# Kernel tuning notes

Measured on AMD Instinct MI355X. Metric: run time of the kernel, lower is better.

## Reference

```python
import jax, jax.numpy as jnp
import numpy as np

R, A, E, K, NREL = 2048, 16384, 131072, 48, 7
RADIUS = 10.0


def setup_inputs():
    key = jax.random.key(0)
    ks = jax.random.split(key, 20)
    f = jax.random.normal
    return {
        "node_feature": f(ks[0], (R, 21), jnp.float32),
        "all_atom_pos": f(ks[1], (A, 3), jnp.float32) * 8.0,
        "atom_name": jax.random.randint(ks[2], (A,), 0, 38),
        "ca_idx": jax.random.randint(ks[3], (R,), 0, A),
        "edge_src": jax.random.randint(ks[4], (E,), 0, R),
        "edge_dst": jax.random.randint(ks[5], (E,), 0, R),
        "edge_rel": jax.random.randint(ks[6], (E,), 0, NREL),
        # parameters (atom-type embedding table, residue-type linear, AEP point MLP,
        # relational graph conv, env2structures MLP with BN)
        "emb_atom": f(ks[7], (39, 64), jnp.float32) * 0.02,
        "Wres": f(ks[8], (21, 64), jnp.float32) * 0.1,
        "bres": jnp.zeros((64,), jnp.float32),
        "Wxyz": f(ks[9], (3, 64), jnp.float32) * 0.1,
        "W1": f(ks[10], (64, 128), jnp.float32) * 0.1,
        "b1": jnp.zeros((128,), jnp.float32),
        "W2": f(ks[11], (128, 256), jnp.float32) * 0.08,
        "b2": jnp.zeros((256,), jnp.float32),
        "Wconv": f(ks[12], (NREL * 64, 512), jnp.float32) * 0.05,
        "bconv": jnp.zeros((512,), jnp.float32),
        "Wself": f(ks[13], (64, 512), jnp.float32) * 0.1,
        "We1": f(ks[14], (512 + 256, 512), jnp.float32) * 0.05,
        "be1": jnp.zeros((512,), jnp.float32),
        "gamma1": jnp.ones((512,), jnp.float32),
        "beta1": jnp.zeros((512,), jnp.float32),
        "We2": f(ks[15], (512, 512), jnp.float32) * 0.05,
        "be2": jnp.zeros((512,), jnp.float32),
    }


def reference(node_feature, all_atom_pos, atom_name, ca_idx, edge_src, edge_dst, edge_rel,
              emb_atom, Wres, bres, Wxyz, W1, b1, W2, b2,
              Wconv, bconv, Wself, We1, be1, gamma1, beta1, We2, be2):
    # residue-type embedding (nn.Linear(21, 64))
    res_feat = node_feature @ Wres + bres                      # [R,64]
    # ball query: each CA gathers all-atom neighbors within RADIUS (fixed K, masked)
    ca = all_atom_pos[ca_idx]                                   # [R,3]
    diff = ca[:, None, :] - all_atom_pos[None, :, :]            # [R,A,3]
    d = jnp.sqrt(jnp.sum(diff * diff, axis=-1) + 1e-12)         # [R,A]
    dm = jnp.where(d < RADIUS, d, jnp.inf)
    negd, nbr = jax.lax.top_k(-dm, K)                           # K nearest in ball
    mask = (-negd) < RADIUS                                     # [R,K]
    maskf = mask.astype(res_feat.dtype)[..., None]
    delta = (all_atom_pos[nbr] - ca[:, None, :]) * maskf        # relative coords [R,K,3]
    # padded atom-type embedding (padding contributes zeros, like padding_idx=38)
    pts = (emb_atom[atom_name[nbr]] + delta @ Wxyz) * maskf     # [R,K,64]
    # AEP point MLP + masked max-pool -> environment feature
    h = jax.nn.relu(pts @ W1 + b1)                              # [R,K,128]
    env = jnp.max(jnp.where(mask[..., None], h, -1e9), axis=1)  # [R,128]
    env = jax.nn.relu(env @ W2 + b2)                            # [R,256]
    # relational graph conv: per-relation scatter-sum over destination nodes
    seg = edge_dst * NREL + edge_rel
    agg = jax.ops.segment_sum(res_feat[edge_src], seg, num_segments=R * NREL)
    agg = agg.reshape(R, NREL * res_feat.shape[1])              # [R, 7*64]
    hres = jax.nn.relu(agg @ Wconv + bconv + res_feat @ Wself)  # [R,512]
    # env2structures MLP (Linear -> BatchNorm1d(train stats) -> ReLU -> Linear)
    z = jnp.concatenate([hres, env], axis=-1) @ We1 + be1       # [R,512]
    z = (z - z.mean(0)) * jax.lax.rsqrt(z.var(0) + 1e-5) * gamma1 + beta1
    return jax.nn.relu(z) @ We2 + be2                           # [R,512]
```

## Files before the change

kernel.cpp:

```cpp
#include <hip/hip_runtime.h>
#include <math.h>

#define R_ 2048
#define A_ 16384
#define E_ 131072
#define K_ 48
#define NREL_ 7

typedef __attribute__((ext_vector_type(8))) short bfrag8;
typedef __attribute__((ext_vector_type(4))) float f32x4v;

__device__ __forceinline__ unsigned short bf16rne(float f) {
    unsigned u = __builtin_bit_cast(unsigned, f);
    u += 0x7FFFu + ((u >> 16) & 1u);
    return (unsigned short)(u >> 16);
}

__global__ __launch_bounds__(256) void k_resfeat(
    const float* __restrict__ node, const float* __restrict__ Wres,
    const float* __restrict__ bres, float* __restrict__ resfeat,
    float* __restrict__ bufA)
{
    int idx = blockIdx.x * 256 + threadIdx.x;
    int r = idx >> 6, c = idx & 63;
    float s = bres[c];
#pragma unroll
    for (int i = 0; i < 21; ++i) s += node[r * 21 + i] * Wres[i * 64 + c];
    resfeat[r * 64 + c] = s;
    bufA[(size_t)r * 512 + 448 + c] = s;
}

__global__ __launch_bounds__(256) void k_prep(
    const float* __restrict__ Wconv, const float* __restrict__ Wself,
    const float* __restrict__ We1, const float* __restrict__ We2,
    unsigned short* __restrict__ Bt1, unsigned short* __restrict__ Bt2,
    unsigned short* __restrict__ Bt3)
{
    int id = blockIdx.x * 256 + threadIdx.x;
    if (id < 262144) {
        int k = id & 511, n = id >> 9;
        float v = (k < 448) ? Wconv[k * 512 + n] : Wself[(k - 448) * 512 + n];
        Bt1[n * 512 + k] = bf16rne(v);
    } else if (id < 655360) {
        int rel = id - 262144;
        int k = rel % 768, n = rel / 768;
        Bt2[n * 768 + k] = bf16rne(We1[k * 512 + n]);
    } else if (id < 917504) {
        int rel = id - 655360;
        int k = rel & 511, n = rel >> 9;
        Bt3[n * 512 + k] = bf16rne(We2[k * 512 + n]);
    }
}

__global__ __launch_bounds__(256) void k_edges(
    const int* __restrict__ esrc, const int* __restrict__ edst,
    const int* __restrict__ erel, const float* __restrict__ resfeat,
    float* __restrict__ bufA)
{
    int idx = blockIdx.x * 256 + threadIdx.x;
    int e = idx >> 6, c = idx & 63;
    int d = edst[e], rel = erel[e], s = esrc[e];
    atomicAdd(&bufA[(size_t)d * 512 + rel * 64 + c], resfeat[s * 64 + c]);
}

__global__ __launch_bounds__(256) void k_ball(
    const float* __restrict__ pos, const int* __restrict__ ca_idx,
    int* __restrict__ nbr)
{
    __shared__ unsigned hist[256];
    __shared__ unsigned hist2[256];
    __shared__ int sc[256];
    __shared__ float candd[128];
    __shared__ int candi[128];
    __shared__ unsigned s_cnt, s_ccnt;
    __shared__ int s_list[64];
    __shared__ int sB, sNeed, sB2, sNeed2, sTotal;

    int tid = threadIdx.x;
    int r = blockIdx.x;
    int ca = ca_idx[r];
    float cx = pos[ca * 3 + 0], cy = pos[ca * 3 + 1], cz = pos[ca * 3 + 2];

    hist[tid] = 0u;
    if (tid == 0) { s_cnt = 0u; s_ccnt = 0u; }
    __syncthreads();

    for (int it = 0; it < 16; ++it) {
        int a0 = it * 1024 + tid * 4;
        const float4* p = (const float4*)(pos + (size_t)a0 * 3);
        float4 p0 = p[0], p1 = p[1], p2 = p[2];
        float xs[4] = { p0.x, p0.w, p1.z, p2.y };
        float ys[4] = { p0.y, p1.x, p1.w, p2.z };
        float zs[4] = { p0.z, p1.y, p2.x, p2.w };
#pragma unroll
        for (int q = 0; q < 4; ++q) {
            float dx = xs[q] - cx, dy = ys[q] - cy, dz = zs[q] - cz;
            float d = sqrtf(dx * dx + dy * dy + dz * dz + 1e-12f);
            if (d < 10.0f) {
                int b = (int)(d * 25.6f); if (b > 255) b = 255;
                atomicAdd(&hist[b], 1u);
            }
        }
    }
    __syncthreads();

    sc[tid] = (int)hist[tid];
    __syncthreads();
    for (int s = 1; s < 256; s <<= 1) {
        int v = (tid >= s) ? sc[tid - s] : 0;
        __syncthreads();
        sc[tid] += v;
        __syncthreads();
    }
    if (tid == 0) sTotal = sc[255];
    if (sc[tid] >= K_ && (tid == 0 || sc[tid - 1] < K_)) {
        sB = tid;
        sNeed = K_ - (sc[tid] - (int)hist[tid]);
    }
    __syncthreads();

    int mode = (sTotal <= K_) ? 0 : (((int)hist[sB] > 128) ? 2 : 1);

    if (mode == 2) {
        int B = sB;
        float lo = B * 0.0390625f;
        hist2[tid] = 0u;
        __syncthreads();
        for (int it = 0; it < 16; ++it) {
            int a0 = it * 1024 + tid * 4;
            const float4* p = (const float4*)(pos + (size_t)a0 * 3);
            float4 p0 = p[0], p1 = p[1], p2 = p[2];
            float xs[4] = { p0.x, p0.w, p1.z, p2.y };
            float ys[4] = { p0.y, p1.x, p1.w, p2.z };
            float zs[4] = { p0.z, p1.y, p2.x, p2.w };
#pragma unroll
            for (int q = 0; q < 4; ++q) {
                float dx = xs[q] - cx, dy = ys[q] - cy, dz = zs[q] - cz;
                float d = sqrtf(dx * dx + dy * dy + dz * dz + 1e-12f);
                if (d < 10.0f) {
                    int b = (int)(d * 25.6f); if (b > 255) b = 255;
                    if (b == B) {
                        int k2 = (int)((d - lo) * 6553.6f);
                        if (k2 < 0) k2 = 0; if (k2 > 255) k2 = 255;
                        atomicAdd(&hist2[k2], 1u);
                    }
                }
            }
        }
        __syncthreads();
        sc[tid] = (int)hist2[tid];
        __syncthreads();
        for (int s = 1; s < 256; s <<= 1) {
            int v = (tid >= s) ? sc[tid - s] : 0;
            __syncthreads();
            sc[tid] += v;
            __syncthreads();
        }
        if (sc[tid] >= sNeed && (tid == 0 || sc[tid - 1] < sNeed)) {
            sB2 = tid;
            sNeed2 = sNeed - (sc[tid] - (int)hist2[tid]);
        }
        __syncthreads();
    }

    {
        int B = (mode == 0) ? 256 : sB;
        float lo = sB * 0.0390625f;
        int B2 = (mode == 2) ? sB2 : 0;
        for (int it = 0; it < 16; ++it) {
            int a0 = it * 1024 + tid * 4;
            const float4* p = (const float4*)(pos + (size_t)a0 * 3);
            float4 p0 = p[0], p1 = p[1], p2 = p[2];
            float xs[4] = { p0.x, p0.w, p1.z, p2.y };
            float ys[4] = { p0.y, p1.x, p1.w, p2.z };
            float zs[4] = { p0.z, p1.y, p2.x, p2.w };
#pragma unroll
            for (int q = 0; q < 4; ++q) {
                int a = a0 + q;
                float dx = xs[q] - cx, dy = ys[q] - cy, dz = zs[q] - cz;
                float d = sqrtf(dx * dx + dy * dy + dz * dz + 1e-12f);
                if (d < 10.0f) {
                    int b = (int)(d * 25.6f); if (b > 255) b = 255;
                    bool take = false, cand = false;
                    if (b < B) take = true;
                    else if (b == B) {
                        if (mode == 1) cand = true;
                        else {
                            int k2 = (int)((d - lo) * 6553.6f);
                            if (k2 < 0) k2 = 0; if (k2 > 255) k2 = 255;
                            if (k2 < B2) take = true;
                            else if (k2 == B2) cand = true;
                        }
                    }
                    if (take) { unsigned pp = atomicAdd(&s_cnt, 1u); s_list[pp] = a; }
                    else if (cand) { unsigned c = atomicAdd(&s_ccnt, 1u); if (c < 128u) { candd[c] = d; candi[c] = a; } }
                }
            }
        }
    }
    __syncthreads();

    int needN = (mode == 0) ? 0 : ((mode == 1) ? sNeed : sNeed2);
    unsigned C = s_ccnt; if (C > 128u) C = 128u;
    if (tid < (int)C) {
        float di = candd[tid]; int ii = candi[tid];
        int rank = 0;
        for (unsigned j = 0; j < C; ++j) {
            float dj = candd[j]; int ij = candi[j];
            if (dj < di || (dj == di && ij < ii)) ++rank;
        }
        if (rank < needN) { unsigned pp = atomicAdd(&s_cnt, 1u); s_list[pp] = ii; }
    }
    __syncthreads();
    if (tid < K_) nbr[r * K_ + tid] = (tid < (int)s_cnt) ? s_list[tid] : -1;
}

__global__ __launch_bounds__(256) void k_env(
    const float* __restrict__ pos, const int* __restrict__ atom_name,
    const int* __restrict__ ca_idx, const int* __restrict__ nbr,
    const float* __restrict__ emb, const float* __restrict__ Wxyz,
    const float* __restrict__ W1, const float* __restrict__ b1,
    const float* __restrict__ W2, const float* __restrict__ b2,
    float* __restrict__ outZ1)
{
    __shared__ __align__(16) float W1s[64 * 128];
    __shared__ __align__(16) float pts[K_ * 64];
    __shared__ float part[8][128];
    __shared__ float env128[128];
    __shared__ int s_a[K_];
    __shared__ float s_d[K_][3];

    int tid = threadIdx.x, r = blockIdx.x;
    for (int i = tid * 4; i < 64 * 128; i += 1024)
        *(float4*)&W1s[i] = *(const float4*)&W1[i];

    int ca = ca_idx[r];
    float cx = pos[ca * 3 + 0], cy = pos[ca * 3 + 1], cz = pos[ca * 3 + 2];
    if (tid < K_) {
        int a = nbr[r * K_ + tid];
        s_a[tid] = a;
        if (a >= 0) {
            s_d[tid][0] = pos[a * 3 + 0] - cx;
            s_d[tid][1] = pos[a * 3 + 1] - cy;
            s_d[tid][2] = pos[a * 3 + 2] - cz;
        } else {
            s_d[tid][0] = 0.f; s_d[tid][1] = 0.f; s_d[tid][2] = 0.f;
        }
    }
    __syncthreads();

    for (int idx = tid; idx < K_ * 64; idx += 256) {
        int k = idx >> 6, i = idx & 63;
        int a = s_a[k];
        float v = 0.f;
        if (a >= 0) {
            v = emb[atom_name[a] * 64 + i]
              + s_d[k][0] * Wxyz[i] + s_d[k][1] * Wxyz[64 + i] + s_d[k][2] * Wxyz[128 + i];
        }
        pts[idx] = v;
    }
    __syncthreads();

    {
        int kg = tid >> 5;
        int j0 = (tid & 31) << 2;
        float acc[6][4];
#pragma unroll
        for (int t = 0; t < 6; ++t)
#pragma unroll
            for (int u = 0; u < 4; ++u) acc[t][u] = 0.f;

        for (int i = 0; i < 64; ++i) {
            float pv[6];
#pragma unroll
            for (int t = 0; t < 6; ++t) pv[t] = pts[(kg * 6 + t) * 64 + i];
            float4 w = *(const float4*)&W1s[i * 128 + j0];
#pragma unroll
            for (int t = 0; t < 6; ++t) {
                acc[t][0] += pv[t] * w.x;
                acc[t][1] += pv[t] * w.y;
                acc[t][2] += pv[t] * w.z;
                acc[t][3] += pv[t] * w.w;
            }
        }
        float4 b1v = *(const float4*)&b1[j0];
        float m[4] = { -1e9f, -1e9f, -1e9f, -1e9f };
#pragma unroll
        for (int t = 0; t < 6; ++t) {
            if (s_a[kg * 6 + t] >= 0) {
                m[0] = fmaxf(m[0], fmaxf(acc[t][0] + b1v.x, 0.f));
                m[1] = fmaxf(m[1], fmaxf(acc[t][1] + b1v.y, 0.f));
                m[2] = fmaxf(m[2], fmaxf(acc[t][2] + b1v.z, 0.f));
                m[3] = fmaxf(m[3], fmaxf(acc[t][3] + b1v.w, 0.f));
            }
        }
#pragma unroll
        for (int u = 0; u < 4; ++u) part[kg][j0 + u] = m[u];
    }
    __syncthreads();
    if (tid < 128) {
        float m = part[0][tid];
#pragma unroll
        for (int g = 1; g < 8; ++g) m = fmaxf(m, part[g][tid]);
        env128[tid] = m;
    }
    __syncthreads();
    {
        float s = b2[tid];
        for (int i = 0; i < 128; ++i) s += env128[i] * W2[i * 256 + tid];
        outZ1[(size_t)r * 768 + 512 + tid] = fmaxf(s, 0.f);
    }
}

__global__ __launch_bounds__(512) void k_stats(
    const float* __restrict__ Z, float* __restrict__ stats)
{
    int j = threadIdx.x;
    int r0 = blockIdx.x * 16;
    float s = 0.f, q = 0.f;
    for (int r = r0; r < r0 + 16; ++r) {
        float v = Z[(size_t)r * 512 + j];
        s += v; q += v * v;
    }
    atomicAdd(&stats[j], s);
    atomicAdd(&stats[512 + j], q);
}

template<bool RELU_OUT, bool BN_A>
__global__ __launch_bounds__(256) void k_mgemm(
    const float* __restrict__ A, int lda, int K,
    const unsigned short* __restrict__ Bt,
    const float* __restrict__ bias,
    const float* __restrict__ stats, const float* __restrict__ gamma,
    const float* __restrict__ beta,
    float* __restrict__ C, int ldc)
{
    __shared__ __align__(16) unsigned short As[32 * 32];
    __shared__ __align__(16) unsigned short Bs[64 * 32];
    __shared__ float bnsc[BN_A ? 512 : 1];
    __shared__ float bnsh[BN_A ? 512 : 1];

    int tid = threadIdx.x;
    int m0 = blockIdx.y * 32, n0 = blockIdx.x * 64;

    if (BN_A) {
        for (int i = tid; i < 512; i += 256) {
            float mean = stats[i] * (1.0f / 2048.0f);
            float var = stats[512 + i] * (1.0f / 2048.0f) - mean * mean;
            float inv = 1.0f / sqrtf(var + 1e-5f);
            float scv = gamma[i] * inv;
            bnsc[i] = scv;
            bnsh[i] = beta[i] - mean * scv;
        }
        __syncthreads();
    }

    int w = tid >> 6, l = tid & 63;
    int wm = w >> 1, wn = w & 1;

    int ar = tid >> 3, ac = tid & 7;
    int aslot = ac >> 1, ahalf = ac & 1;
    int abyte = ar * 64 + ((aslot ^ ((ar >> 1) & 3)) << 4) + ahalf * 8;
    int bn_ = tid >> 2, bs_ = tid & 3;
    int bbyte = bn_ * 64 + ((bs_ ^ ((bn_ >> 1) & 3)) << 4);

    int fr = l & 15, fo = l >> 4;
    int arow = 16 * wm + fr;
    int afbyte = arow * 64 + ((fo ^ ((arow >> 1) & 3)) << 4);
    int bcol0 = 32 * wn + fr;
    int bfbyte0 = bcol0 * 64 + ((fo ^ ((bcol0 >> 1) & 3)) << 4);
    int bcol1 = bcol0 + 16;
    int bfbyte1 = bcol1 * 64 + ((fo ^ ((bcol1 >> 1) & 3)) << 4);

    f32x4v acc0 = { 0.f, 0.f, 0.f, 0.f };
    f32x4v acc1 = { 0.f, 0.f, 0.f, 0.f };

    for (int k0 = 0; k0 < K; k0 += 32) {
        float4 av = *(const float4*)(A + (size_t)(m0 + ar) * lda + k0 + ac * 4);
        uint4 bv = *(const uint4*)(Bt + (size_t)(n0 + bn_) * K + k0 + bs_ * 8);
        if (BN_A) {
            int kb = k0 + ac * 4;
            av.x = fmaxf(av.x * bnsc[kb + 0] + bnsh[kb + 0], 0.f);
            av.y = fmaxf(av.y * bnsc[kb + 1] + bnsh[kb + 1], 0.f);
            av.z = fmaxf(av.z * bnsc[kb + 2] + bnsh[kb + 2], 0.f);
            av.w = fmaxf(av.w * bnsc[kb + 3] + bnsh[kb + 3], 0.f);
        }
        unsigned lo = (unsigned)bf16rne(av.x) | ((unsigned)bf16rne(av.y) << 16);
        unsigned hi = (unsigned)bf16rne(av.z) | ((unsigned)bf16rne(av.w) << 16);
        __syncthreads();
        *(uint2*)((char*)As + abyte) = make_uint2(lo, hi);
        *(uint4*)((char*)Bs + bbyte) = bv;
        __syncthreads();

        bfrag8 af = *(const bfrag8*)((const char*)As + afbyte);
        bfrag8 bf0 = *(const bfrag8*)((const char*)Bs + bfbyte0);
        bfrag8 bf1 = *(const bfrag8*)((const char*)Bs + bfbyte1);
        acc0 = __builtin_amdgcn_mfma_f32_16x16x32_bf16(af, bf0, acc0, 0, 0, 0);
        acc1 = __builtin_amdgcn_mfma_f32_16x16x32_bf16(af, bf1, acc1, 0, 0, 0);
    }

    int col0 = n0 + 32 * wn + fr;
    int row = m0 + 16 * wm + fo * 4;
    float bb0 = bias[col0], bb1 = bias[col0 + 16];
#pragma unroll
    for (int i = 0; i < 4; ++i) {
        float v0 = acc0[i] + bb0;
        float v1 = acc1[i] + bb1;
        if (RELU_OUT) { v0 = fmaxf(v0, 0.f); v1 = fmaxf(v1, 0.f); }
        C[(size_t)(row + i) * ldc + col0] = v0;
        C[(size_t)(row + i) * ldc + col0 + 16] = v1;
    }
}

extern "C" void kernel_launch(void* const* d_in, const int* in_sizes, int n_in,
                              void* d_out, int out_size, void* d_ws, size_t ws_size,
                              hipStream_t stream)
{
    const float* node   = (const float*)d_in[0];
    const float* pos    = (const float*)d_in[1];
    const int*   aname  = (const int*)d_in[2];
    const int*   caidx  = (const int*)d_in[3];
    const int*   esrc   = (const int*)d_in[4];
    const int*   edst   = (const int*)d_in[5];
    const int*   erel   = (const int*)d_in[6];
    const float* emb    = (const float*)d_in[7];
    const float* Wres   = (const float*)d_in[8];
    const float* bres   = (const float*)d_in[9];
    const float* Wxyz   = (const float*)d_in[10];
    const float* W1     = (const float*)d_in[11];
    const float* b1     = (const float*)d_in[12];
    const float* W2     = (const float*)d_in[13];
    const float* b2     = (const float*)d_in[14];
    const float* Wconv  = (const float*)d_in[15];
    const float* bconv  = (const float*)d_in[16];
    const float* Wself  = (const float*)d_in[17];
    const float* We1    = (const float*)d_in[18];
    const float* be1    = (const float*)d_in[19];
    const float* gamma1 = (const float*)d_in[20];
    const float* beta1  = (const float*)d_in[21];
    const float* We2    = (const float*)d_in[22];
    const float* be2    = (const float*)d_in[23];
    float* out = (float*)d_out;

    char* ws = (char*)d_ws;
    float* resfeat = (float*)(ws + 0);
    float* bufA    = (float*)(ws + 524288);
    float* bufZ1   = (float*)(ws + 4718592);
    float* bufZ2   = (float*)(ws + 11010048);
    int*   nbr     = (int*)  (ws + 15204352);
    float* stats   = (float*)(ws + 15597568);
    unsigned short* Bt1 = (unsigned short*)(ws + 15601664);
    unsigned short* Bt2 = (unsigned short*)(ws + 16125952);
    unsigned short* Bt3 = (unsigned short*)(ws + 16912384);

    hipMemsetAsync(bufA, 0, (size_t)R_ * 512 * 4, stream);
    hipMemsetAsync(stats, 0, 1024 * 4, stream);

    k_prep<<<3584, 256, 0, stream>>>(Wconv, Wself, We1, We2, Bt1, Bt2, Bt3);
    k_resfeat<<<R_ * 64 / 256, 256, 0, stream>>>(node, Wres, bres, resfeat, bufA);
    k_ball<<<R_, 256, 0, stream>>>(pos, caidx, nbr);
    k_env<<<R_, 256, 0, stream>>>(pos, aname, caidx, nbr, emb, Wxyz, W1, b1, W2, b2, bufZ1);
    k_edges<<<(size_t)E_ * 64 / 256, 256, 0, stream>>>(esrc, edst, erel, resfeat, bufA);

    dim3 gg(512 / 64, R_ / 32);
    k_mgemm<true, false><<<gg, 256, 0, stream>>>(
        bufA, 512, 512, Bt1, bconv, nullptr, nullptr, nullptr, bufZ1, 768);
    k_mgemm<false, false><<<gg, 256, 0, stream>>>(
        bufZ1, 768, 768, Bt2, be1, nullptr, nullptr, nullptr, bufZ2, 512);
    k_stats<<<R_ / 16, 512, 0, stream>>>(bufZ2, stats);
    k_mgemm<false, true><<<gg, 256, 0, stream>>>(
        bufZ2, 512, 512, Bt3, be2, stats, gamma1, beta1, out, 512);
}
```

Before: 273.9 us.

## Cache ball-query bins, use MFMA for point MLP, fuse stats and prep kernels

Several independent changes land together. The ball query now bins by squared distance and caches the per-atom bin indices in shared memory, so the later passes no longer reread positions or recompute sqrt; exact distances are only computed for boundary candidates. The env kernel's 64x128 point MLP moves from scalar FP32 FMAs to bf16 MFMA using a pre-transposed W1, and the max-pool reduces with wave shuffles. BatchNorm statistics are accumulated in the second GEMM's epilogue instead of a separate kernel, and the residue embedding is merged into the prep kernel. These cut launches and redundant memory passes, at the cost of bf16 rounding in the point MLP and bin boundaries that now differ slightly in squared-distance space.

```diff
diff --git a/kernel.cpp b/kernel.cpp
--- a/kernel.cpp
+++ b/kernel.cpp
@@ -16,25 +16,21 @@
     return (unsigned short)(u >> 16);
 }
 
-__global__ __launch_bounds__(256) void k_resfeat(
-    const float* __restrict__ node, const float* __restrict__ Wres,
-    const float* __restrict__ bres, float* __restrict__ resfeat,
-    float* __restrict__ bufA)
-{
-    int idx = blockIdx.x * 256 + threadIdx.x;
-    int r = idx >> 6, c = idx & 63;
-    float s = bres[c];
-#pragma unroll
-    for (int i = 0; i < 21; ++i) s += node[r * 21 + i] * Wres[i * 64 + c];
-    resfeat[r * 64 + c] = s;
-    bufA[(size_t)r * 512 + 448 + c] = s;
+__device__ __forceinline__ float dist2(float x, float y, float z,
+                                       float cx, float cy, float cz) {
+    float dx = x - cx, dy = y - cy, dz = z - cz;
+    return fmaf(dx, dx, fmaf(dy, dy, dz * dz));
 }
 
 __global__ __launch_bounds__(256) void k_prep(
     const float* __restrict__ Wconv, const float* __restrict__ Wself,
     const float* __restrict__ We1, const float* __restrict__ We2,
+    const float* __restrict__ W1,
+    const float* __restrict__ node, const float* __restrict__ Wres,
+    const float* __restrict__ bres,
     unsigned short* __restrict__ Bt1, unsigned short* __restrict__ Bt2,
-    unsigned short* __restrict__ Bt3)
+    unsigned short* __restrict__ Bt3, unsigned short* __restrict__ W1t,
+    float* __restrict__ resfeat, float* __restrict__ bufA)
 {
     int id = blockIdx.x * 256 + threadIdx.x;
     if (id < 262144) {
@@ -49,6 +45,18 @@
         int rel = id - 655360;
         int k = rel & 511, n = rel >> 9;
         Bt3[n * 512 + k] = bf16rne(We2[k * 512 + n]);
+    } else if (id < 925696) {
+        int rel = id - 917504;
+        int k = rel & 63, n = rel >> 6;
+        W1t[n * 64 + k] = bf16rne(W1[k * 128 + n]);
+    } else if (id < 1056768) {
+        int rel = id - 925696;
+        int r = rel >> 6, c = rel & 63;
+        float s = bres[c];
+#pragma unroll
+        for (int i = 0; i < 21; ++i) s += node[r * 21 + i] * Wres[i * 64 + c];
+        resfeat[r * 64 + c] = s;
+        bufA[(size_t)r * 512 + 448 + c] = s;
     }
 }
 
@@ -67,6 +75,7 @@
     const float* __restrict__ pos, const int* __restrict__ ca_idx,
     int* __restrict__ nbr)
 {
+    __shared__ unsigned binsw[4096];
     __shared__ unsigned hist[256];
     __shared__ unsigned hist2[256];
     __shared__ int sc[256];
@@ -92,15 +101,18 @@
         float xs[4] = { p0.x, p0.w, p1.z, p2.y };
         float ys[4] = { p0.y, p1.x, p1.w, p2.z };
         float zs[4] = { p0.z, p1.y, p2.x, p2.w };
+        unsigned pack = 0;
 #pragma unroll
         for (int q = 0; q < 4; ++q) {
-            float dx = xs[q] - cx, dy = ys[q] - cy, dz = zs[q] - cz;
-            float d = sqrtf(dx * dx + dy * dy + dz * dz + 1e-12f);
-            if (d < 10.0f) {
-                int b = (int)(d * 25.6f); if (b > 255) b = 255;
+            float d2 = dist2(xs[q], ys[q], zs[q], cx, cy, cz);
+            int b = 255;
+            if (d2 < 100.0f) {
+                b = (int)(d2 * 2.56f); if (b > 254) b = 254;
                 atomicAdd(&hist[b], 1u);
             }
-        }
+            pack |= (unsigned)b << (q * 8);
+        }
+        binsw[it * 256 + tid] = pack;
     }
     __syncthreads();
 
@@ -121,29 +133,37 @@
 
     int mode = (sTotal <= K_) ? 0 : (((int)hist[sB] > 128) ? 2 : 1);
 
-    if (mode == 2) {
+    if (mode <= 1) {
+        int B = (mode == 0) ? 255 : sB;
+        for (int it = 0; it < 16; ++it) {
+            unsigned pack = binsw[it * 256 + tid];
+            int a0 = it * 1024 + tid * 4;
+#pragma unroll
+            for (int q = 0; q < 4; ++q) {
+                int b = (pack >> (q * 8)) & 255;
+                if (b < B) { unsigned pp = atomicAdd(&s_cnt, 1u); s_list[pp] = a0 + q; }
+                else if (b == B && mode == 1) {
+                    unsigned c = atomicAdd(&s_ccnt, 1u);
+                    if (c < 128u) candi[c] = a0 + q;
+                }
+            }
+        }
+    } else {
         int B = sB;
-        float lo = B * 0.0390625f;
+        float lo2 = B * 0.390625f;
         hist2[tid] = 0u;
         __syncthreads();
         for (int it = 0; it < 16; ++it) {
+            unsigned pack = binsw[it * 256 + tid];
             int a0 = it * 1024 + tid * 4;
-            const float4* p = (const float4*)(pos + (size_t)a0 * 3);
-            float4 p0 = p[0], p1 = p[1], p2 = p[2];
-            float xs[4] = { p0.x, p0.w, p1.z, p2.y };
-            float ys[4] = { p0.y, p1.x, p1.w, p2.z };
-            float zs[4] = { p0.z, p1.y, p2.x, p2.w };
 #pragma unroll
             for (int q = 0; q < 4; ++q) {
-                float dx = xs[q] - cx, dy = ys[q] - cy, dz = zs[q] - cz;
-                float d = sqrtf(dx * dx + dy * dy + dz * dz + 1e-12f);
-                if (d < 10.0f) {
-                    int b = (int)(d * 25.6f); if (b > 255) b = 255;
-                    if (b == B) {
-                        int k2 = (int)((d - lo) * 6553.6f);
-                        if (k2 < 0) k2 = 0; if (k2 > 255) k2 = 255;
-                        atomicAdd(&hist2[k2], 1u);
-                    }
+                if (((pack >> (q * 8)) & 255) == (unsigned)B) {
+                    int a = a0 + q;
+                    float d2 = dist2(pos[a * 3], pos[a * 3 + 1], pos[a * 3 + 2], cx, cy, cz);
+                    int k2 = (int)((d2 - lo2) * 655.36f);
+                    if (k2 < 0) k2 = 0; if (k2 > 255) k2 = 255;
+                    atomicAdd(&hist2[k2], 1u);
                 }
             }
         }
@@ -161,39 +181,24 @@
             sNeed2 = sNeed - (sc[tid] - (int)hist2[tid]);
         }
         __syncthreads();
-    }
-
-    {
-        int B = (mode == 0) ? 256 : sB;
-        float lo = sB * 0.0390625f;
-        int B2 = (mode == 2) ? sB2 : 0;
+        int B2 = sB2;
         for (int it = 0; it < 16; ++it) {
+            unsigned pack = binsw[it * 256 + tid];
             int a0 = it * 1024 + tid * 4;
-            const float4* p = (const float4*)(pos + (size_t)a0 * 3);
-            float4 p0 = p[0], p1 = p[1], p2 = p[2];
-            float xs[4] = { p0.x, p0.w, p1.z, p2.y };
-            float ys[4] = { p0.y, p1.x, p1.w, p2.z };
-            float zs[4] = { p0.z, p1.y, p2.x, p2.w };
 #pragma unroll
             for (int q = 0; q < 4; ++q) {
-                int a = a0 + q;
-                float dx = xs[q] - cx, dy = ys[q] - cy, dz = zs[q] - cz;
-                float d = sqrtf(dx * dx + dy * dy + dz * dz + 1e-12f);
-                if (d < 10.0f) {
-                    int b = (int)(d * 25.6f); if (b > 255) b = 255;
-                    bool take = false, cand = false;
-                    if (b < B) take = true;
-                    else if (b == B) {
-                        if (mode == 1) cand = true;
-                        else {
-                            int k2 = (int)((d - lo) * 6553.6f);
-                            if (k2 < 0) k2 = 0; if (k2 > 255) k2 = 255;
-                            if (k2 < B2) take = true;
-                            else if (k2 == B2) cand = true;
-                        }
+                int b = (pack >> (q * 8)) & 255;
+                if (b < B) { unsigned pp = atomicAdd(&s_cnt, 1u); s_list[pp] = a0 + q; }
+                else if (b == B) {
+                    int a = a0 + q;
+                    float d2 = dist2(pos[a * 3], pos[a * 3 + 1], pos[a * 3 + 2], cx, cy, cz);
+                    int k2 = (int)((d2 - lo2) * 655.36f);
+                    if (k2 < 0) k2 = 0; if (k2 > 255) k2 = 255;
+                    if (k2 < B2) { unsigned pp = atomicAdd(&s_cnt, 1u); s_list[pp] = a; }
+                    else if (k2 == B2) {
+                        unsigned c = atomicAdd(&s_ccnt, 1u);
+                        if (c < 128u) candi[c] = a;
                     }
-                    if (take) { unsigned pp = atomicAdd(&s_cnt, 1u); s_list[pp] = a; }
-                    else if (cand) { unsigned c = atomicAdd(&s_ccnt, 1u); if (c < 128u) { candd[c] = d; candi[c] = a; } }
                 }
             }
         }
@@ -202,6 +207,12 @@
 
     int needN = (mode == 0) ? 0 : ((mode == 1) ? sNeed : sNeed2);
     unsigned C = s_ccnt; if (C > 128u) C = 128u;
+    if (tid < (int)C) {
+        int a = candi[tid];
+        float d2 = dist2(pos[a * 3], pos[a * 3 + 1], pos[a * 3 + 2], cx, cy, cz);
+        candd[tid] = sqrtf(d2 + 1e-12f);
+    }
+    __syncthreads();
     if (tid < (int)C) {
         float di = candd[tid]; int ii = candi[tid];
         int rank = 0;
@@ -219,20 +230,24 @@
     const float* __restrict__ pos, const int* __restrict__ atom_name,
     const int* __restrict__ ca_idx, const int* __restrict__ nbr,
     const float* __restrict__ emb, const float* __restrict__ Wxyz,
-    const float* __restrict__ W1, const float* __restrict__ b1,
+    const unsigned short* __restrict__ W1t,
+    const float* __restrict__ b1,
     const float* __restrict__ W2, const float* __restrict__ b2,
     float* __restrict__ outZ1)
 {
-    __shared__ __align__(16) float W1s[64 * 128];
-    __shared__ __align__(16) float pts[K_ * 64];
-    __shared__ float part[8][128];
+    __shared__ __align__(16) float pts[48 * 68];
+    __shared__ __align__(16) unsigned short W1s[128 * 72];
     __shared__ float env128[128];
-    __shared__ int s_a[K_];
-    __shared__ float s_d[K_][3];
+    __shared__ float sWxyz[192];
+    __shared__ float s_d[48][3];
+    __shared__ int s_a[48];
+    __shared__ int s_an[48];
 
     int tid = threadIdx.x, r = blockIdx.x;
-    for (int i = tid * 4; i < 64 * 128; i += 1024)
-        *(float4*)&W1s[i] = *(const float4*)&W1[i];
+
+    for (int c = tid; c < 1024; c += 256)
+        *(uint4*)((char*)W1s + (c >> 3) * 144 + (c & 7) * 16) = ((const uint4*)W1t)[c];
+    if (tid < 192) sWxyz[tid] = Wxyz[tid];
 
     int ca = ca_idx[r];
     float cx = pos[ca * 3 + 0], cy = pos[ca * 3 + 1], cz = pos[ca * 3 + 2];
@@ -243,68 +258,82 @@
             s_d[tid][0] = pos[a * 3 + 0] - cx;
             s_d[tid][1] = pos[a * 3 + 1] - cy;
             s_d[tid][2] = pos[a * 3 + 2] - cz;
+            s_an[tid] = atom_name[a];
         } else {
             s_d[tid][0] = 0.f; s_d[tid][1] = 0.f; s_d[tid][2] = 0.f;
+            s_an[tid] = 0;
         }
     }
     __syncthreads();
 
     for (int idx = tid; idx < K_ * 64; idx += 256) {
-        int k = idx >> 6, i = idx & 63;
-        int a = s_a[k];
+        int row = idx >> 6, k = idx & 63;
+        int a = s_a[row];
         float v = 0.f;
         if (a >= 0) {
-            v = emb[atom_name[a] * 64 + i]
-              + s_d[k][0] * Wxyz[i] + s_d[k][1] * Wxyz[64 + i] + s_d[k][2] * Wxyz[128 + i];
-        }
-        pts[idx] = v;
-    }
-    __syncthreads();
-
-    {
-        int kg = tid >> 5;
-        int j0 = (tid & 31) << 2;
-        float acc[6][4];
-#pragma unroll
-        for (int t = 0; t < 6; ++t)
-#pragma unroll
-            for (int u = 0; u < 4; ++u) acc[t][u] = 0.f;
-
-        for (int i = 0; i < 64; ++i) {
-            float pv[6];
-#pragma unroll
-            for (int t = 0; t < 6; ++t) pv[t] = pts[(kg * 6 + t) * 64 + i];
-            float4 w = *(const float4*)&W1s[i * 128 + j0];
-#pragma unroll
-            for (int t = 0; t < 6; ++t) {
-                acc[t][0] += pv[t] * w.x;
-                acc[t][1] += pv[t] * w.y;
-                acc[t][2] += pv[t] * w.z;
-                acc[t][3] += pv[t] * w.w;
+            v = emb[s_an[row] * 64 + k]
+              + s_d[row][0] * sWxyz[k] + s_d[row][1] * sWxyz[64 + k]
+              + s_d[row][2] * sWxyz[128 + k];
+        }
+        pts[row * 68 + k] = v;
+    }
+    __syncthreads();
+
+    int w = tid >> 6, l = tid & 63;
+    int fr = l & 15, fo = l >> 4;
+    f32x4v acc[3][2];
+#pragma unroll
+    for (int m = 0; m < 3; ++m)
+#pragma unroll
+        for (int n = 0; n < 2; ++n) acc[m][n] = (f32x4v){0.f, 0.f, 0.f, 0.f};
+
+#pragma unroll
+    for (int ks = 0; ks < 2; ++ks) {
+        bfrag8 af[3], bf[2];
+#pragma unroll
+        for (int m = 0; m < 3; ++m) {
+            int row = 16 * m + fr;
+            const char* base = (const char*)pts + row * 272 + ks * 128 + fo * 32;
+            float4 v0 = *(const float4*)base;
+            float4 v1 = *(const float4*)(base + 16);
+            bfrag8 t;
+            t[0] = (short)bf16rne(v0.x); t[1] = (short)bf16rne(v0.y);
+            t[2] = (short)bf16rne(v0.z); t[3] = (short)bf16rne(v0.w);
+            t[4] = (short)bf16rne(v1.x); t[5] = (short)bf16rne(v1.y);
+            t[6] = (short)bf16rne(v1.z); t[7] = (short)bf16rne(v1.w);
+            af[m] = t;
+        }
+#pragma unroll
+        for (int n = 0; n < 2; ++n) {
+            int wrow = (2 * w + n) * 16 + fr;
+            bf[n] = *(const bfrag8*)((const char*)W1s + wrow * 144 + ks * 64 + fo * 16);
+        }
+#pragma unroll
+        for (int m = 0; m < 3; ++m)
+#pragma unroll
+            for (int n = 0; n < 2; ++n)
+                acc[m][n] = __builtin_amdgcn_mfma_f32_16x16x32_bf16(af[m], bf[n], acc[m][n], 0, 0, 0);
+    }
+
+#pragma unroll
+    for (int n = 0; n < 2; ++n) {
+        int col = 32 * w + n * 16 + fr;
+        float bv = b1[col];
+        float m = -1e30f;
+#pragma unroll
+        for (int mt = 0; mt < 3; ++mt) {
+#pragma unroll
+            for (int i = 0; i < 4; ++i) {
+                int row = 16 * mt + fo * 4 + i;
+                if (s_a[row] >= 0) m = fmaxf(m, fmaxf(acc[mt][n][i] + bv, 0.f));
             }
         }
-        float4 b1v = *(const float4*)&b1[j0];
-        float m[4] = { -1e9f, -1e9f, -1e9f, -1e9f };
-#pragma unroll
-        for (int t = 0; t < 6; ++t) {
-            if (s_a[kg * 6 + t] >= 0) {
-                m[0] = fmaxf(m[0], fmaxf(acc[t][0] + b1v.x, 0.f));
-                m[1] = fmaxf(m[1], fmaxf(acc[t][1] + b1v.y, 0.f));
-                m[2] = fmaxf(m[2], fmaxf(acc[t][2] + b1v.z, 0.f));
-                m[3] = fmaxf(m[3], fmaxf(acc[t][3] + b1v.w, 0.f));
-            }
-        }
-#pragma unroll
-        for (int u = 0; u < 4; ++u) part[kg][j0 + u] = m[u];
-    }
-    __syncthreads();
-    if (tid < 128) {
-        float m = part[0][tid];
-#pragma unroll
-        for (int g = 1; g < 8; ++g) m = fmaxf(m, part[g][tid]);
-        env128[tid] = m;
-    }
-    __syncthreads();
+        m = fmaxf(m, __shfl_xor(m, 16));
+        m = fmaxf(m, __shfl_xor(m, 32));
+        if (fo == 0 && (l & 48) == 0) env128[col] = m;
+    }
+    __syncthreads();
+
     {
         float s = b2[tid];
         for (int i = 0; i < 128; ++i) s += env128[i] * W2[i * 256 + tid];
@@ -312,28 +341,14 @@
     }
 }
 
-__global__ __launch_bounds__(512) void k_stats(
-    const float* __restrict__ Z, float* __restrict__ stats)
-{
-    int j = threadIdx.x;
-    int r0 = blockIdx.x * 16;
-    float s = 0.f, q = 0.f;
-    for (int r = r0; r < r0 + 16; ++r) {
-        float v = Z[(size_t)r * 512 + j];
-        s += v; q += v * v;
-    }
-    atomicAdd(&stats[j], s);
-    atomicAdd(&stats[512 + j], q);
-}
-
-template<bool RELU_OUT, bool BN_A>
+template<bool RELU_OUT, bool BN_A, bool STATS>
 __global__ __launch_bounds__(256) void k_mgemm(
     const float* __restrict__ A, int lda, int K,
     const unsigned short* __restrict__ Bt,
     const float* __restrict__ bias,
     const float* __restrict__ stats, const float* __restrict__ gamma,
     const float* __restrict__ beta,
-    float* __restrict__ C, int ldc)
+    float* __restrict__ C, int ldc, float* __restrict__ statsOut)
 {
     __shared__ __align__(16) unsigned short As[32 * 32];
     __shared__ __align__(16) unsigned short Bs[64 * 32];
@@ -402,13 +417,27 @@
     int col0 = n0 + 32 * wn + fr;
     int row = m0 + 16 * wm + fo * 4;
     float bb0 = bias[col0], bb1 = bias[col0 + 16];
+    float s0 = 0.f, q0 = 0.f, s1 = 0.f, q1 = 0.f;
 #pragma unroll
     for (int i = 0; i < 4; ++i) {
         float v0 = acc0[i] + bb0;
         float v1 = acc1[i] + bb1;
         if (RELU_OUT) { v0 = fmaxf(v0, 0.f); v1 = fmaxf(v1, 0.f); }
+        if (STATS) { s0 += v0; q0 += v0 * v0; s1 += v1; q1 += v1 * v1; }
         C[(size_t)(row + i) * ldc + col0] = v0;
         C[(size_t)(row + i) * ldc + col0 + 16] = v1;
+    }
+    if (STATS) {
+        s0 += __shfl_xor(s0, 16); s0 += __shfl_xor(s0, 32);
+        q0 += __shfl_xor(q0, 16); q0 += __shfl_xor(q0, 32);
+        s1 += __shfl_xor(s1, 16); s1 += __shfl_xor(s1, 32);
+        q1 += __shfl_xor(q1, 16); q1 += __shfl_xor(q1, 32);
+        if (fo == 0 && (l & 48) == 0) {
+            atomicAdd(&statsOut[col0], s0);
+            atomicAdd(&statsOut[512 + col0], q0);
+            atomicAdd(&statsOut[col0 + 16], s1);
+            atomicAdd(&statsOut[512 + col0 + 16], q1);
+        }
     }
 }
 
@@ -452,22 +481,22 @@
     unsigned short* Bt1 = (unsigned short*)(ws + 15601664);
     unsigned short* Bt2 = (unsigned short*)(ws + 16125952);
     unsigned short* Bt3 = (unsigned short*)(ws + 16912384);
+    unsigned short* W1t = (unsigned short*)(ws + 17436672);
 
     hipMemsetAsync(bufA, 0, (size_t)R_ * 512 * 4, stream);
     hipMemsetAsync(stats, 0, 1024 * 4, stream);
 
-    k_prep<<<3584, 256, 0, stream>>>(Wconv, Wself, We1, We2, Bt1, Bt2, Bt3);
-    k_resfeat<<<R_ * 64 / 256, 256, 0, stream>>>(node, Wres, bres, resfeat, bufA);
+    k_prep<<<4128, 256, 0, stream>>>(Wconv, Wself, We1, We2, W1, node, Wres, bres,
+                                     Bt1, Bt2, Bt3, W1t, resfeat, bufA);
     k_ball<<<R_, 256, 0, stream>>>(pos, caidx, nbr);
-    k_env<<<R_, 256, 0, stream>>>(pos, aname, caidx, nbr, emb, Wxyz, W1, b1, W2, b2, bufZ1);
+    k_env<<<R_, 256, 0, stream>>>(pos, aname, caidx, nbr, emb, Wxyz, W1t, b1, W2, b2, bufZ1);
     k_edges<<<(size_t)E_ * 64 / 256, 256, 0, stream>>>(esrc, edst, erel, resfeat, bufA);
 
     dim3 gg(512 / 64, R_ / 32);
-    k_mgemm<true, false><<<gg, 256, 0, stream>>>(
-        bufA, 512, 512, Bt1, bconv, nullptr, nullptr, nullptr, bufZ1, 768);
-    k_mgemm<false, false><<<gg, 256, 0, stream>>>(
-        bufZ1, 768, 768, Bt2, be1, nullptr, nullptr, nullptr, bufZ2, 512);
-    k_stats<<<R_ / 16, 512, 0, stream>>>(bufZ2, stats);
-    k_mgemm<false, true><<<gg, 256, 0, stream>>>(
-        bufZ2, 512, 512, Bt3, be2, stats, gamma1, beta1, out, 512);
-}
+    k_mgemm<true, false, false><<<gg, 256, 0, stream>>>(
+        bufA, 512, 512, Bt1, bconv, nullptr, nullptr, nullptr, bufZ1, 768, nullptr);
+    k_mgemm<false, false, true><<<gg, 256, 0, stream>>>(
+        bufZ1, 768, 768, Bt2, be1, nullptr, nullptr, nullptr, bufZ2, 512, stats);
+    k_mgemm<false, true, false><<<gg, 256, 0, stream>>>(
+        bufZ2, 512, 512, Bt3, be2, stats, gamma1, beta1, out, 512, nullptr);
+}
```

New measurement: 234.2 us. -14.5%, faster.
